# Kernel optimization log

Hardware: AMD Instinct MI355X
Metric: run time of the kernel (lower is better)

## Reference

```python
import jax, jax.numpy as jnp
import numpy as np

B, LQ, LKV, D = 32, 1024, 1024, 512

def setup_inputs() -> dict:
    key = jax.random.key(0)
    kq, kkv = jax.random.split(key)
    query = jax.random.normal(kq, (B, LQ, D), dtype=jnp.float32)
    key_value = jax.random.normal(kkv, (B, LKV, D), dtype=jnp.float32)
    return {"query": query, "key_value": key_value}

def reference(query, key_value):
    # scores: [B, Lq, Lkv] (unscaled dot-product attention)
    scores = jnp.einsum('bqd,bkd->bqk', query, key_value)
    attn_score = jax.nn.softmax(scores, axis=-1)
    # output: [B, Lq, D]
    output = jnp.einsum('bqk,bkd->bqd', attn_score, key_value)
    return (output, attn_score)
```

## Files before the change

### kernel.cpp

```cpp
#include <hip/hip_runtime.h>


constexpr int NB  = 32;
constexpr int LQ  = 1024;
constexpr int LKV = 1024;
constexpr int DD  = 512;

typedef __attribute__((ext_vector_type(4))) float f4;
typedef __attribute__((ext_vector_type(4))) float f32x4;
typedef __attribute__((ext_vector_type(4))) unsigned short u16x4;
typedef __attribute__((ext_vector_type(8))) __bf16 bf16x8;

__device__ __forceinline__ unsigned short f2bf(float x) {
  unsigned u = __builtin_bit_cast(unsigned, x);
  unsigned r = u + 0x7FFFu + ((u >> 16) & 1u);
  return (unsigned short)(r >> 16);
}
__device__ __forceinline__ float bf2f(unsigned short h) {
  unsigned u = ((unsigned)h) << 16;
  return __builtin_bit_cast(float, u);
}

__device__ __forceinline__ void gload16(const void* g, void* l) {
  __builtin_amdgcn_global_load_lds((const __attribute__((address_space(1))) unsigned int*)g,
                                   (__attribute__((address_space(3))) unsigned int*)l,
                                   16, 0, 0);
}

constexpr int PAD = 40;

__global__ __launch_bounds__(256) void qsplit_kernel(const float* __restrict__ Q,
                                                     unsigned short* __restrict__ Qh,
                                                     unsigned short* __restrict__ Ql)
{
  const size_t N = (size_t)NB * LQ * DD;
  for (size_t i = ((size_t)blockIdx.x * 256 + threadIdx.x) * 4; i < N;
       i += (size_t)gridDim.x * 256 * 4) {
    f4 v = *(const f4*)(Q + i);
    u16x4 h, l;
#pragma unroll
    for (int u = 0; u < 4; ++u) {
      h[u] = f2bf(v[u]);
      l[u] = f2bf(v[u] - bf2f(h[u]));
    }
    *(u16x4*)(Qh + i) = h;
    *(u16x4*)(Ql + i) = l;
  }
}

__global__ __launch_bounds__(256) void kvt_prep2_kernel(const float* __restrict__ KV,
                                                        unsigned short* __restrict__ Kh,
                                                        unsigned short* __restrict__ Kl,
                                                        unsigned short* __restrict__ KVT)
{
  __shared__ unsigned short T[64][72];
  const int b  = blockIdx.z;
  const int tk = blockIdx.y;
  const int td = blockIdx.x;
  const int tid = threadIdx.x;

#pragma unroll
  for (int i = 0; i < 4; ++i) {
    int idx = tid + i * 256;
    int r   = idx >> 4;
    int c4  = (idx & 15) << 2;
    size_t goff = ((size_t)b * LKV + tk * 64 + r) * DD + td * 64 + c4;
    f4 v = *(const f4*)(KV + goff);
    u16x4 h, l;
#pragma unroll
    for (int u = 0; u < 4; ++u) {
      h[u] = f2bf(v[u]);
      l[u] = f2bf(v[u] - bf2f(h[u]));
    }
    *(u16x4*)&T[r][c4] = h;
    *(u16x4*)(Kh + goff) = h;
    *(u16x4*)(Kl + goff) = l;
  }
  __syncthreads();

#pragma unroll
  for (int i = 0; i < 4; ++i) {
    int idx = tid + i * 256;
    int c   = idx >> 4;
    int r4  = (idx & 15) << 2;
    u16x4 w = { T[r4][c], T[r4 + 1][c], T[r4 + 2][c], T[r4 + 3][c] };
    *(u16x4*)(KVT + ((size_t)b * DD + td * 64 + c) * LKV + tk * 64 + r4) = w;
  }
}

__global__ __launch_bounds__(256) void gemm_qk3_kernel(const unsigned short* __restrict__ Qh,
                                                       const unsigned short* __restrict__ Ql,
                                                       const unsigned short* __restrict__ Kh,
                                                       const unsigned short* __restrict__ Kl,
                                                       float* __restrict__ S)
{
  __shared__ unsigned short SM[4][128 * 64];
  const int b   = blockIdx.y;
  const int ti  = blockIdx.x >> 3;
  const int tj  = blockIdx.x & 7;
  const int tid  = threadIdx.x;
  const int lane = tid & 63;
  const int wid  = tid >> 6;
  const int wr = (wid >> 1) * 64;
  const int wc = (wid & 1) * 64;

  const size_t qo = ((size_t)b * LQ  + ti * 128) * DD;
  const size_t ko = ((size_t)b * LKV + tj * 128) * DD;
  const unsigned short* tb =
      (wid == 0) ? Qh + qo : (wid == 1) ? Ql + qo : (wid == 2) ? Kh + ko : Kl + ko;

  const int lrow = lane >> 3;
  const int ss   = (lane & 7) ^ lrow;

  f32x4 acc[4][4] = {};

  for (int ks = 0; ks < DD; ks += 64) {
    __syncthreads();
#pragma unroll
    for (int i = 0; i < 16; ++i) {
      const unsigned short* g = tb + (size_t)(i * 8 + lrow) * DD + ks + ss * 8;
      gload16(g, &SM[wid][i * 512]);
    }
    __syncthreads();

#pragma unroll
    for (int kk = 0; kk < 64; kk += 32) {
      const int cl  = (kk + ((lane >> 4) << 3)) >> 3;
      const int sp8 = (cl ^ (lane & 7)) * 8;
      bf16x8 ah[4], al[4], bh[4], bl[4];
#pragma unroll
      for (int m = 0; m < 4; ++m) {
        int r = wr + m * 16 + (lane & 15);
        ah[m] = *(const bf16x8*)&SM[0][r * 64 + sp8];
        al[m] = *(const bf16x8*)&SM[1][r * 64 + sp8];
      }
#pragma unroll
      for (int n = 0; n < 4; ++n) {
        int r = wc + n * 16 + (lane & 15);
        bh[n] = *(const bf16x8*)&SM[2][r * 64 + sp8];
        bl[n] = *(const bf16x8*)&SM[3][r * 64 + sp8];
      }
#pragma unroll
      for (int m = 0; m < 4; ++m)
#pragma unroll
        for (int n = 0; n < 4; ++n)
          acc[m][n] = __builtin_amdgcn_mfma_f32_16x16x32_bf16(ah[m], bh[n], acc[m][n], 0, 0, 0);
#pragma unroll
      for (int m = 0; m < 4; ++m)
#pragma unroll
        for (int n = 0; n < 4; ++n)
          acc[m][n] = __builtin_amdgcn_mfma_f32_16x16x32_bf16(ah[m], bl[n], acc[m][n], 0, 0, 0);
#pragma unroll
      for (int m = 0; m < 4; ++m)
#pragma unroll
        for (int n = 0; n < 4; ++n)
          acc[m][n] = __builtin_amdgcn_mfma_f32_16x16x32_bf16(al[m], bh[n], acc[m][n], 0, 0, 0);
    }
  }

  float* Sb = S + (size_t)b * LQ * LKV;
#pragma unroll
  for (int m = 0; m < 4; ++m) {
    int row0 = ti * 128 + wr + m * 16 + ((lane >> 4) << 2);
#pragma unroll
    for (int n = 0; n < 4; ++n) {
      int col = tj * 128 + wc + n * 16 + (lane & 15);
#pragma unroll
      for (int j = 0; j < 4; ++j)
        Sb[(size_t)(row0 + j) * LKV + col] = acc[m][n][j];
    }
  }
}

__global__ __launch_bounds__(256) void gemm_qk_kernel(const float* __restrict__ Q,
                                                      const float* __restrict__ KV,
                                                      float* __restrict__ S)
{
  __shared__ unsigned short Ah[128][PAD], Al[128][PAD], Bh[128][PAD], Bl[128][PAD];
  const int b   = blockIdx.y;
  const int ti  = blockIdx.x >> 3;
  const int tj  = blockIdx.x & 7;
  const int tid  = threadIdx.x;
  const int lane = tid & 63;
  const int wid  = tid >> 6;
  const int wr = (wid >> 1) * 64;
  const int wc = (wid & 1) * 64;

  const float* Qb = Q  + (size_t)b * LQ  * DD + (size_t)ti * 128 * DD;
  const float* Kb = KV + (size_t)b * LKV * DD + (size_t)tj * 128 * DD;

  f32x4 acc[4][4] = {};

  for (int ks = 0; ks < DD; ks += 32) {
    __syncthreads();
#pragma unroll
    for (int i = 0; i < 4; ++i) {
      int idx = tid + i * 256;
      int r   = idx >> 3;
      int k4  = (idx & 7) << 2;
      f4 qa = *(const f4*)(Qb + (size_t)r * DD + ks + k4);
      f4 ka = *(const f4*)(Kb + (size_t)r * DD + ks + k4);
      u16x4 qh, ql, kh, kl;
#pragma unroll
      for (int u = 0; u < 4; ++u) {
        unsigned short h = f2bf(qa[u]);
        qh[u] = h;  ql[u] = f2bf(qa[u] - bf2f(h));
        unsigned short h2 = f2bf(ka[u]);
        kh[u] = h2; kl[u] = f2bf(ka[u] - bf2f(h2));
      }
      *(u16x4*)&Ah[r][k4] = qh;  *(u16x4*)&Al[r][k4] = ql;
      *(u16x4*)&Bh[r][k4] = kh;  *(u16x4*)&Bl[r][k4] = kl;
    }
    __syncthreads();

    const int kf = (lane >> 4) << 3;
    bf16x8 ah[4], al[4], bh[4], bl[4];
#pragma unroll
    for (int m = 0; m < 4; ++m) {
      int row = wr + m * 16 + (lane & 15);
      ah[m] = *(const bf16x8*)&Ah[row][kf];
      al[m] = *(const bf16x8*)&Al[row][kf];
    }
#pragma unroll
    for (int n = 0; n < 4; ++n) {
      int row = wc + n * 16 + (lane & 15);
      bh[n] = *(const bf16x8*)&Bh[row][kf];
      bl[n] = *(const bf16x8*)&Bl[row][kf];
    }
#pragma unroll
    for (int m = 0; m < 4; ++m)
#pragma unroll
      for (int n = 0; n < 4; ++n) {
        acc[m][n] = __builtin_amdgcn_mfma_f32_16x16x32_bf16(ah[m], bh[n], acc[m][n], 0, 0, 0);
        acc[m][n] = __builtin_amdgcn_mfma_f32_16x16x32_bf16(ah[m], bl[n], acc[m][n], 0, 0, 0);
        acc[m][n] = __builtin_amdgcn_mfma_f32_16x16x32_bf16(al[m], bh[n], acc[m][n], 0, 0, 0);
      }
  }

  float* Sb = S + (size_t)b * LQ * LKV;
#pragma unroll
  for (int m = 0; m < 4; ++m) {
    int row0 = ti * 128 + wr + m * 16 + ((lane >> 4) << 2);
#pragma unroll
    for (int n = 0; n < 4; ++n) {
      int col = tj * 128 + wc + n * 16 + (lane & 15);
#pragma unroll
      for (int j = 0; j < 4; ++j)
        Sb[(size_t)(row0 + j) * LKV + col] = acc[m][n][j];
    }
  }
}

__global__ __launch_bounds__(256) void softmax_kernel(float* __restrict__ S)
{
  __shared__ float redmax[4], redsum[4];
  const int tid = threadIdx.x;
  float* p = S + (size_t)blockIdx.x * LKV;

  f4 v = *(const f4*)(p + tid * 4);
  float mx = fmaxf(fmaxf(v[0], v[1]), fmaxf(v[2], v[3]));
#pragma unroll
  for (int off = 32; off >= 1; off >>= 1)
    mx = fmaxf(mx, __shfl_xor(mx, off));
  if ((tid & 63) == 0) redmax[tid >> 6] = mx;
  __syncthreads();
  mx = fmaxf(fmaxf(redmax[0], redmax[1]), fmaxf(redmax[2], redmax[3]));

  f4 e;
#pragma unroll
  for (int u = 0; u < 4; ++u) e[u] = __expf(v[u] - mx);
  float sm = e[0] + e[1] + e[2] + e[3];
#pragma unroll
  for (int off = 32; off >= 1; off >>= 1)
    sm += __shfl_xor(sm, off);
  if ((tid & 63) == 0) redsum[tid >> 6] = sm;
  __syncthreads();
  sm = redsum[0] + redsum[1] + redsum[2] + redsum[3];

  float inv = 1.0f / sm;
  f4 o = { e[0] * inv, e[1] * inv, e[2] * inv, e[3] * inv };
  *(f4*)(p + tid * 4) = o;
}

__global__ __launch_bounds__(256) void kvt_prep_kernel(const float* __restrict__ KV,
                                                       unsigned short* __restrict__ KVT)
{
  __shared__ unsigned short T[64][72];
  const int b  = blockIdx.z;
  const int tk = blockIdx.y;
  const int td = blockIdx.x;
  const int tid = threadIdx.x;

#pragma unroll
  for (int i = 0; i < 4; ++i) {
    int idx = tid + i * 256;
    int r   = idx >> 4;
    int c4  = (idx & 15) << 2;
    f4 v = *(const f4*)(KV + ((size_t)b * LKV + tk * 64 + r) * DD + td * 64 + c4);
    u16x4 h;
#pragma unroll
    for (int u = 0; u < 4; ++u) h[u] = f2bf(v[u]);
    *(u16x4*)&T[r][c4] = h;
  }
  __syncthreads();

#pragma unroll
  for (int i = 0; i < 4; ++i) {
    int idx = tid + i * 256;
    int c   = idx >> 4;
    int r4  = (idx & 15) << 2;
    u16x4 w = { T[r4][c], T[r4 + 1][c], T[r4 + 2][c], T[r4 + 3][c] };
    *(u16x4*)(KVT + ((size_t)b * DD + td * 64 + c) * LKV + tk * 64 + r4) = w;
  }
}

__global__ __launch_bounds__(512) void gemm_av2_kernel(const float* __restrict__ A,
                                                       const unsigned short* __restrict__ KVT,
                                                       float* __restrict__ O)
{
  __shared__ unsigned short Asm[128][72];
  __shared__ unsigned short Bsm[256 * 64];
  const int b  = blockIdx.z;
  const int mi = blockIdx.y;
  const int nj = blockIdx.x;
  const int tid  = threadIdx.x;
  const int lane = tid & 63;
  const int wid  = tid >> 6;
  const int wr = (wid >> 2) * 64;
  const int wc = (wid & 3) * 64;

  const float* Ab = A + (size_t)b * LQ * LKV + (size_t)mi * 128 * LKV;
  const unsigned short* Bb = KVT + ((size_t)b * DD + nj * 256) * LKV;

  f32x4 acc[4][4] = {};

  for (int ks = 0; ks < LKV; ks += 64) {
    __syncthreads();
#pragma unroll
    for (int i = 0; i < 4; ++i) {
      int idx = tid + i * 512;
      int r   = idx >> 4;
      int k4  = (idx & 15) << 2;
      f4 v = *(const f4*)(Ab + (size_t)r * LKV + ks + k4);
      u16x4 h;
#pragma unroll
      for (int u = 0; u < 4; ++u) h[u] = f2bf(v[u]);
      *(u16x4*)&Asm[r][k4] = h;
    }
#pragma unroll
    for (int c = 0; c < 4; ++c) {
      int cc = wid * 4 + c;
      int dd = cc * 8 + (lane >> 3);
      int ss = (lane & 7) ^ (dd & 7);
      const unsigned short* g = Bb + (size_t)dd * LKV + ks + ss * 8;
      gload16(g, &Bsm[cc * 512]);
    }
    __syncthreads();

#pragma unroll
    for (int kk = 0; kk < 64; kk += 32) {
      const int kf = kk + ((lane >> 4) << 3);
      const int cl = kf >> 3;
      bf16x8 af[4], bfv[4];
#pragma unroll
      for (int m = 0; m < 4; ++m)
        af[m] = *(const bf16x8*)&Asm[wr + m * 16 + (lane & 15)][kf];
#pragma unroll
      for (int n = 0; n < 4; ++n) {
        int dd = wc + n * 16 + (lane & 15);
        int sp = cl ^ (dd & 7);
        bfv[n] = *(const bf16x8*)&Bsm[dd * 64 + sp * 8];
      }
#pragma unroll
      for (int m = 0; m < 4; ++m)
#pragma unroll
        for (int n = 0; n < 4; ++n)
          acc[m][n] = __builtin_amdgcn_mfma_f32_16x16x32_bf16(af[m], bfv[n], acc[m][n], 0, 0, 0);
    }
  }

  float* Ob = O + (size_t)b * LQ * DD;
#pragma unroll
  for (int m = 0; m < 4; ++m) {
    int row0 = mi * 128 + wr + m * 16 + ((lane >> 4) << 2);
#pragma unroll
    for (int n = 0; n < 4; ++n) {
      int col = nj * 256 + wc + n * 16 + (lane & 15);
#pragma unroll
      for (int j = 0; j < 4; ++j)
        Ob[(size_t)(row0 + j) * DD + col] = acc[m][n][j];
    }
  }
}

__global__ __launch_bounds__(256) void gemm_av_kernel(const float* __restrict__ A,
                                                      const float* __restrict__ KV,
                                                      float* __restrict__ O)
{
  __shared__ unsigned short Ab[128][PAD], Bt[128][PAD];
  const int b  = blockIdx.z;
  const int mi = blockIdx.y;
  const int nj = blockIdx.x;
  const int tid  = threadIdx.x;
  const int lane = tid & 63;
  const int wid  = tid >> 6;
  const int wr = (wid >> 1) * 64;
  const int wc = (wid & 1) * 64;

  const float* Arow = A  + (size_t)b * LQ * LKV + (size_t)mi * 128 * LKV;
  const float* Kb   = KV + (size_t)b * LKV * DD;

  f32x4 acc[4][4] = {};

  for (int ks = 0; ks < LKV; ks += 32) {
    __syncthreads();
#pragma unroll
    for (int i = 0; i < 4; ++i) {
      int idx = tid + i * 256;
      {
        int r  = idx >> 3;
        int k4 = (idx & 7) << 2;
        f4 av = *(const f4*)(Arow + (size_t)r * LKV + ks + k4);
        u16x4 h;
#pragma unroll
        for (int u = 0; u < 4; ++u) h[u] = f2bf(av[u]);
        *(u16x4*)&Ab[r][k4] = h;
      }
      {
        int kr = idx >> 5;
        int c4 = (idx & 31) << 2;
        f4 kv = *(const f4*)(Kb + (size_t)(ks + kr) * DD + nj * 128 + c4);
        unsigned short hv[4];
#pragma unroll
        for (int u = 0; u < 4; ++u) hv[u] = f2bf(kv[u]);
#pragma unroll
        for (int u = 0; u < 4; ++u) {
          int uu = (u + kr) & 3;
          Bt[c4 + uu][kr] = hv[uu];
        }
      }
    }
    __syncthreads();

    const int kf = (lane >> 4) << 3;
    bf16x8 af[4], bfv[4];
#pragma unroll
    for (int m = 0; m < 4; ++m)
      af[m] = *(const bf16x8*)&Ab[wr + m * 16 + (lane & 15)][kf];
#pragma unroll
    for (int n = 0; n < 4; ++n)
      bfv[n] = *(const bf16x8*)&Bt[wc + n * 16 + (lane & 15)][kf];
#pragma unroll
    for (int m = 0; m < 4; ++m)
#pragma unroll
      for (int n = 0; n < 4; ++n)
        acc[m][n] = __builtin_amdgcn_mfma_f32_16x16x32_bf16(af[m], bfv[n], acc[m][n], 0, 0, 0);
  }

  float* Ob = O + (size_t)b * LQ * DD;
#pragma unroll
  for (int m = 0; m < 4; ++m) {
    int row0 = mi * 128 + wr + m * 16 + ((lane >> 4) << 2);
#pragma unroll
    for (int n = 0; n < 4; ++n) {
      int col = nj * 128 + wc + n * 16 + (lane & 15);
#pragma unroll
      for (int j = 0; j < 4; ++j)
        Ob[(size_t)(row0 + j) * DD + col] = acc[m][n][j];
    }
  }
}

extern "C" void kernel_launch(void* const* d_in, const int* in_sizes, int n_in,
                              void* d_out, int out_size, void* d_ws, size_t ws_size,
                              hipStream_t stream) {
  const float* Q  = (const float*)d_in[0];
  const float* KV = (const float*)d_in[1];
  float* out  = (float*)d_out;
  float* attn = out + (size_t)NB * LQ * DD;

  const size_t NQ  = (size_t)NB * LQ * DD;
  const size_t big_bytes = 5 * NQ * sizeof(unsigned short);
  const size_t kvt_bytes = NQ * sizeof(unsigned short);

  if (ws_size >= big_bytes) {
    unsigned short* Qh  = (unsigned short*)d_ws;
    unsigned short* Qlo = Qh  + NQ;
    unsigned short* Kh  = Qlo + NQ;
    unsigned short* Kl  = Kh  + NQ;
    unsigned short* KVT = Kl  + NQ;
    qsplit_kernel<<<4096, 256, 0, stream>>>(Q, Qh, Qlo);
    kvt_prep2_kernel<<<dim3(DD / 64, LKV / 64, NB), 256, 0, stream>>>(KV, Kh, Kl, KVT);
    gemm_qk3_kernel<<<dim3(64, NB), 256, 0, stream>>>(Qh, Qlo, Kh, Kl, attn);
    softmax_kernel<<<dim3(NB * LQ), 256, 0, stream>>>(attn);
    gemm_av2_kernel<<<dim3(DD / 256, LQ / 128, NB), 512, 0, stream>>>(attn, KVT, out);
  } else if (ws_size >= kvt_bytes) {
    unsigned short* KVT = (unsigned short*)d_ws;
    gemm_qk_kernel<<<dim3(64, NB), 256, 0, stream>>>(Q, KV, attn);
    kvt_prep_kernel<<<dim3(DD / 64, LKV / 64, NB), 256, 0, stream>>>(KV, KVT);
    softmax_kernel<<<dim3(NB * LQ), 256, 0, stream>>>(attn);
    gemm_av2_kernel<<<dim3(DD / 256, LQ / 128, NB), 512, 0, stream>>>(attn, KVT, out);
  } else {
    gemm_qk_kernel<<<dim3(64, NB), 256, 0, stream>>>(Q, KV, attn);
    softmax_kernel<<<dim3(NB * LQ), 256, 0, stream>>>(attn);
    gemm_av_kernel<<<dim3(DD / 128, LQ / 128, NB), 256, 0, stream>>>(attn, KV, out);
  }
}
```

Baseline: 290.8 us.

## Fuse softmax into QK epilogue stats and AV prologue; merge prep kernels

Result: slower. 334.0 us (+14.9%).

```diff
diff --git a/kernel.cpp b/kernel.cpp
--- a/kernel.cpp
+++ b/kernel.cpp
@@ -5,6 +5,7 @@
 constexpr int LQ  = 1024;
 constexpr int LKV = 1024;
 constexpr int DD  = 512;
+constexpr int NROWS = NB * LQ;
 
 typedef __attribute__((ext_vector_type(4))) float f4;
 typedef __attribute__((ext_vector_type(4))) float f32x4;
@@ -29,29 +30,13 @@
 
 constexpr int PAD = 40;
 
-__global__ __launch_bounds__(256) void qsplit_kernel(const float* __restrict__ Q,
-                                                     unsigned short* __restrict__ Qh,
-                                                     unsigned short* __restrict__ Ql)
-{
-  const size_t N = (size_t)NB * LQ * DD;
-  for (size_t i = ((size_t)blockIdx.x * 256 + threadIdx.x) * 4; i < N;
-       i += (size_t)gridDim.x * 256 * 4) {
-    f4 v = *(const f4*)(Q + i);
-    u16x4 h, l;
-#pragma unroll
-    for (int u = 0; u < 4; ++u) {
-      h[u] = f2bf(v[u]);
-      l[u] = f2bf(v[u] - bf2f(h[u]));
-    }
-    *(u16x4*)(Qh + i) = h;
-    *(u16x4*)(Ql + i) = l;
-  }
-}
-
-__global__ __launch_bounds__(256) void kvt_prep2_kernel(const float* __restrict__ KV,
-                                                        unsigned short* __restrict__ Kh,
-                                                        unsigned short* __restrict__ Kl,
-                                                        unsigned short* __restrict__ KVT)
+__global__ __launch_bounds__(256) void prep_all_kernel(const float* __restrict__ Q,
+                                                       const float* __restrict__ KV,
+                                                       unsigned short* __restrict__ Qh,
+                                                       unsigned short* __restrict__ Ql,
+                                                       unsigned short* __restrict__ Kh,
+                                                       unsigned short* __restrict__ Kl,
+                                                       unsigned short* __restrict__ KVT)
 {
   __shared__ unsigned short T[64][72];
   const int b  = blockIdx.z;
@@ -75,6 +60,16 @@
     *(u16x4*)&T[r][c4] = h;
     *(u16x4*)(Kh + goff) = h;
     *(u16x4*)(Kl + goff) = l;
+
+    f4 q = *(const f4*)(Q + goff);
+    u16x4 qh, ql;
+#pragma unroll
+    for (int u = 0; u < 4; ++u) {
+      qh[u] = f2bf(q[u]);
+      ql[u] = f2bf(q[u] - bf2f(qh[u]));
+    }
+    *(u16x4*)(Qh + goff) = qh;
+    *(u16x4*)(Ql + goff) = ql;
   }
   __syncthreads();
 
@@ -88,11 +83,13 @@
   }
 }
 
-__global__ __launch_bounds__(256) void gemm_qk3_kernel(const unsigned short* __restrict__ Qh,
+__global__ __launch_bounds__(256) void gemm_qk4_kernel(const unsigned short* __restrict__ Qh,
                                                        const unsigned short* __restrict__ Ql,
                                                        const unsigned short* __restrict__ Kh,
                                                        const unsigned short* __restrict__ Kl,
-                                                       float* __restrict__ S)
+                                                       float* __restrict__ S,
+                                                       float* __restrict__ Pmax,
+                                                       float* __restrict__ Psum)
 {
   __shared__ unsigned short SM[4][128 * 64];
   const int b   = blockIdx.y;
@@ -168,6 +165,144 @@
 #pragma unroll
       for (int j = 0; j < 4; ++j)
         Sb[(size_t)(row0 + j) * LKV + col] = acc[m][n][j];
+    }
+  }
+
+  const int g16  = lane >> 4;
+  const int l16  = lane & 15;
+  const int wcid = wc >> 6;
+#pragma unroll
+  for (int m = 0; m < 4; ++m) {
+#pragma unroll
+    for (int j = 0; j < 4; ++j) {
+      float rm = fmaxf(fmaxf(acc[m][0][j], acc[m][1][j]), fmaxf(acc[m][2][j], acc[m][3][j]));
+#pragma unroll
+      for (int off = 8; off >= 1; off >>= 1)
+        rm = fmaxf(rm, __shfl_xor(rm, off));
+      float se = 0.f;
+#pragma unroll
+      for (int n = 0; n < 4; ++n)
+        se += __expf(acc[m][n][j] - rm);
+#pragma unroll
+      for (int off = 8; off >= 1; off >>= 1)
+        se += __shfl_xor(se, off);
+      if (l16 == 0) {
+        int row  = ti * 128 + wr + m * 16 + g16 * 4 + j;
+        size_t p = ((size_t)b * LQ + row) * 16 + tj * 2 + wcid;
+        Pmax[p] = rm;
+        Psum[p] = se;
+      }
+    }
+  }
+}
+
+__global__ __launch_bounds__(256) void reduce_stats_kernel(const float* __restrict__ Pmax,
+                                                           const float* __restrict__ Psum,
+                                                           float* __restrict__ M,
+                                                           float* __restrict__ Inv)
+{
+  int row = blockIdx.x * 256 + threadIdx.x;
+  const float* pm = Pmax + (size_t)row * 16;
+  const float* ps = Psum + (size_t)row * 16;
+  float mx = pm[0];
+#pragma unroll
+  for (int i = 1; i < 16; ++i) mx = fmaxf(mx, pm[i]);
+  float s = 0.f;
+#pragma unroll
+  for (int i = 0; i < 16; ++i) s += ps[i] * __expf(pm[i] - mx);
+  M[row]   = mx;
+  Inv[row] = 1.0f / s;
+}
+
+__global__ __launch_bounds__(512) void gemm_av6_kernel(float* __restrict__ Sio,
+                                                       const unsigned short* __restrict__ KVT,
+                                                       const float* __restrict__ Mrow,
+                                                       const float* __restrict__ Invr,
+                                                       float* __restrict__ O)
+{
+  __shared__ unsigned short Asm[64][72];
+  __shared__ unsigned short Bsm[512 * 64];
+  __shared__ float Ms[64], Is[64];
+  const int b  = blockIdx.y;
+  const int mi = blockIdx.x;
+  const int tid  = threadIdx.x;
+  const int lane = tid & 63;
+  const int wid  = tid >> 6;
+
+  float* Sb = Sio + ((size_t)b * LQ + mi * 64) * LKV;
+  const unsigned short* Bb = KVT + (size_t)b * DD * LKV;
+
+  if (tid < 64) {
+    int gr = b * LQ + mi * 64 + tid;
+    Ms[tid] = Mrow[gr];
+    Is[tid] = Invr[gr];
+  }
+
+  const int lrow = lane >> 3;
+  const int ssw  = (lane & 7) ^ lrow;
+
+  f32x4 acc[4][4] = {};
+
+  for (int ks = 0; ks < LKV; ks += 64) {
+    __syncthreads();
+#pragma unroll
+    for (int i = 0; i < 2; ++i) {
+      int idx = tid + i * 512;
+      int r   = idx >> 4;
+      int k4  = (idx & 15) << 2;
+      float* ap = Sb + (size_t)r * LKV + ks + k4;
+      f4 v = *(const f4*)ap;
+      f4 p; u16x4 h;
+      float mr = Ms[r], ir = Is[r];
+#pragma unroll
+      for (int u = 0; u < 4; ++u) {
+        p[u] = __expf(v[u] - mr) * ir;
+        h[u] = f2bf(p[u]);
+      }
+      *(f4*)ap = p;
+      *(u16x4*)&Asm[r][k4] = h;
+    }
+#pragma unroll
+    for (int c = 0; c < 8; ++c) {
+      int cc = wid * 8 + c;
+      int dd = cc * 8 + lrow;
+      const unsigned short* g = Bb + (size_t)dd * LKV + ks + ssw * 8;
+      gload16(g, &Bsm[cc * 512]);
+    }
+    __syncthreads();
+
+#pragma unroll
+    for (int kk = 0; kk < 64; kk += 32) {
+      const int kf = kk + ((lane >> 4) << 3);
+      const int cl = kf >> 3;
+      bf16x8 af[4], bfv[4];
+#pragma unroll
+      for (int m = 0; m < 4; ++m)
+        af[m] = *(const bf16x8*)&Asm[m * 16 + (lane & 15)][kf];
+#pragma unroll
+      for (int n = 0; n < 4; ++n) {
+        int dd = wid * 64 + n * 16 + (lane & 15);
+        int sp = cl ^ (dd & 7);
+        bfv[n] = *(const bf16x8*)&Bsm[dd * 64 + sp * 8];
+      }
+#pragma unroll
+      for (int m = 0; m < 4; ++m)
+#pragma unroll
+        for (int n = 0; n < 4; ++n)
+          acc[m][n] = __builtin_amdgcn_mfma_f32_16x16x32_bf16(af[m], bfv[n], acc[m][n], 0, 0, 0);
+    }
+  }
+
+  float* Ob = O + ((size_t)b * LQ + mi * 64) * DD;
+#pragma unroll
+  for (int m = 0; m < 4; ++m) {
+    int r0 = m * 16 + ((lane >> 4) << 2);
+#pragma unroll
+    for (int n = 0; n < 4; ++n) {
+      int col = wid * 64 + n * 16 + (lane & 15);
+#pragma unroll
+      for (int j = 0; j < 4; ++j)
+        Ob[(size_t)(r0 + j) * DD + col] = acc[m][n][j];
     }
   }
 }
@@ -489,11 +624,15 @@
     unsigned short* Kh  = Qlo + NQ;
     unsigned short* Kl  = Kh  + NQ;
     unsigned short* KVT = Kl  + NQ;
-    qsplit_kernel<<<4096, 256, 0, stream>>>(Q, Qh, Qlo);
-    kvt_prep2_kernel<<<dim3(DD / 64, LKV / 64, NB), 256, 0, stream>>>(KV, Kh, Kl, KVT);
-    gemm_qk3_kernel<<<dim3(64, NB), 256, 0, stream>>>(Qh, Qlo, Kh, Kl, attn);
-    softmax_kernel<<<dim3(NB * LQ), 256, 0, stream>>>(attn);
-    gemm_av2_kernel<<<dim3(DD / 256, LQ / 128, NB), 512, 0, stream>>>(attn, KVT, out);
+    float* Pmax = out;
+    float* Psum = out + (size_t)NROWS * 16;
+    float* Mrow = (float*)Kh;
+    float* Invr = Mrow + NROWS;
+
+    prep_all_kernel<<<dim3(DD / 64, LKV / 64, NB), 256, 0, stream>>>(Q, KV, Qh, Qlo, Kh, Kl, KVT);
+    gemm_qk4_kernel<<<dim3(64, NB), 256, 0, stream>>>(Qh, Qlo, Kh, Kl, attn, Pmax, Psum);
+    reduce_stats_kernel<<<NROWS / 256, 256, 0, stream>>>(Pmax, Psum, Mrow, Invr);
+    gemm_av6_kernel<<<dim3(LQ / 64, NB), 512, 0, stream>>>(attn, KVT, Mrow, Invr, out);
   } else if (ws_size >= kvt_bytes) {
     unsigned short* KVT = (unsigned short*)d_ws;
     gemm_qk_kernel<<<dim3(64, NB), 256, 0, stream>>>(Q, KV, attn);
```
